# Kernel optimization log

Hardware: AMD Instinct MI355X
Metric: run time of the kernel (lower is better)

Reference implementation:

```python
import jax, jax.numpy as jnp
import numpy as np

# kernel hyperparameters (base_params)
NUGGET = 0.001
REG_LAMBDA = 0.01
FIT_L, FIT_SIGMA = 1.0, 1.0
MMD_L, MMD_SIGMA = 1.0, 1.0
N, D = 4096, 4


def rbf_gram(X1, X2, l, sigma):
    # [N1,N2] radial kernel: sigma^2 * exp(-||x-x'||^2 / (2 l^2)), vectorized
    sq = (jnp.sum(X1 * X1, axis=1)[:, None]
          + jnp.sum(X2 * X2, axis=1)[None, :]
          - 2.0 * (X1 @ X2.T))
    sq = jnp.maximum(sq, 0.0)
    return (sigma * sigma) * jnp.exp(-sq / (2.0 * l * l))


def setup_inputs() -> dict:
    key = jax.random.key(0)
    kx, ky, kz = jax.random.split(key, 3)
    X = jax.random.normal(kx, (N, D), dtype=jnp.float32)
    Y = jax.random.normal(ky, (N, D), dtype=jnp.float32)
    Z = Y + 0.1 * jax.random.normal(kz, (N, D), dtype=jnp.float32)  # Z init'd from Y, perturbed
    return {"X": X, "Y": Y, "Z": Z}


def reference(X, Y, Z):
    # fit_kXX and its nugget-regularized inverse (precomputed in __init__)
    fit_kXX = rbf_gram(X, X, FIT_L, FIT_SIGMA)
    fit_kXX_inv = jnp.linalg.inv(fit_kXX + NUGGET * jnp.eye(X.shape[0], dtype=X.dtype))

    # loss_fit_z: ||k_ZZ||_F^2 - 2 ||k_ZY||_F^2  (torch matrix norm = Frobenius)
    k_ZZ = rbf_gram(Z, Z, MMD_L, MMD_SIGMA)
    k_ZY = rbf_gram(Z, Y, MMD_L, MMD_SIGMA)
    loss_fit = jnp.sum(k_ZZ * k_ZZ) - 2.0 * jnp.sum(k_ZY * k_ZY)

    # loss_reg_z: reg_lambda * trace(Z^T fit_kXX_inv Z)
    loss_reg = REG_LAMBDA * jnp.sum(Z * (fit_kXX_inv @ Z))

    return loss_fit + loss_reg
```

## Files before the change

kernel.cpp:

```cpp
#include <hip/hip_runtime.h>


#define NN 4096
#define LDA 4100
#define OFF_W   ((size_t)NN*LDA)
#define OFF_ACC (OFF_W + (size_t)NN*4)

__device__ __forceinline__ float rdlane(float v, int l){
    return __int_as_float(__builtin_amdgcn_readlane(__float_as_int(v), l));
}

__device__ void wave_chol64(const float* Dm, float* __restrict__ A, int h){
    const int lane = threadIdx.x & 63;
    float row[64];
#pragma unroll
    for (int q=0;q<16;q++){
        float4 v = *(const float4*)(Dm + lane*68 + q*4);
        row[q*4]=v.x; row[q*4+1]=v.y; row[q*4+2]=v.z; row[q*4+3]=v.w;
    }
#pragma unroll
    for (int j=0;j<64;j++){
        float d  = rdlane(row[j], j);
        float sd = sqrtf(d);
        float inv= 1.0f/sd;
        float v  = (lane==j)? sd : row[j]*inv;
        row[j] = v;
#pragma unroll
        for (int c=j+1;c<64;c++){
            float lc = rdlane(v, c);
            row[c] -= v*lc;
        }
    }
#pragma unroll
    for (int q=0;q<16;q++)
        *(float4*)(A + (size_t)(h+lane)*LDA + h + q*4) =
            make_float4(row[q*4],row[q*4+1],row[q*4+2],row[q*4+3]);
}

__global__ void k_build_A(const float* __restrict__ X, float* __restrict__ A){
    const int i  = blockIdx.y;
    const int j0 = (blockIdx.x*256 + threadIdx.x)*4;
    const float4 xi = *(const float4*)(X + (size_t)i*4);
    float out[4];
#pragma unroll
    for (int s=0;s<4;s++){
        const float4 xj = *(const float4*)(X + (size_t)(j0+s)*4);
        float d0=xi.x-xj.x, d1=xi.y-xj.y, d2=xi.z-xj.z, d3=xi.w-xj.w;
        float sq = d0*d0+d1*d1+d2*d2+d3*d3;
        float v  = __expf(-0.5f*sq);
        if (i == j0+s) v += 0.001f;
        out[s]=v;
    }
    *(float4*)(A + (size_t)i*LDA + j0) = make_float4(out[0],out[1],out[2],out[3]);
}

__global__ void k_init(const float* __restrict__ Z, float* __restrict__ W,
                       double* __restrict__ acc){
    const int i = blockIdx.x*256+threadIdx.x;
    ((float4*)W)[i] = ((const float4*)Z)[i];
    if (blockIdx.x==0 && threadIdx.x==0) acc[0]=0.0;
}

__global__ __launch_bounds__(256) void k_chol0(float* __restrict__ A){
    __shared__ float Dm[64*68];
    const int tid = threadIdx.x;
#pragma unroll
    for (int it=0; it<4; ++it){
        int idx = tid + it*256, r = idx>>4, q = idx&15;
        float4 v = *(const float4*)(A + (size_t)r*LDA + q*4);
        *(float4*)&Dm[r*68 + q*4] = v;
    }
    __syncthreads();
    if (tid < 64) wave_chol64(Dm, A, 0);
}

__global__ __launch_bounds__(256) void k_trsm2(float* __restrict__ A, float* __restrict__ W,
                                               int g){
    __shared__ float Ld[64*68];
    __shared__ float dinv[64];
    const int tid = threadIdx.x;
    const int s0  = g*64;
#pragma unroll
    for (int it=0; it<4; ++it){
        int idx = tid + it*256, r = idx>>4, q = idx&15;
        float4 v = *(const float4*)(A + (size_t)(s0+r)*LDA + s0 + q*4);
        *(float4*)&Ld[r*68 + q*4] = v;
    }
    __syncthreads();
    if (tid < 64) dinv[tid] = 1.0f/Ld[tid*68 + tid];
    __syncthreads();

    const int nRB = (66-g)>>2;
    if ((int)blockIdx.x < nRB){
        const int row = s0 + 64 + blockIdx.x*256 + tid;
        const int rl  = row>4095 ? 4095 : row;
        float x[64];
        const float* src = A + (size_t)rl*LDA + s0;
#pragma unroll
        for (int q=0;q<16;q++){
            float4 v = *(const float4*)(src + q*4);
            x[q*4]=v.x; x[q*4+1]=v.y; x[q*4+2]=v.z; x[q*4+3]=v.w;
        }
#pragma unroll
        for (int c=0;c<64;c++){
            float xc = x[c]*dinv[c];
            x[c] = xc;
#pragma unroll
            for (int t=c+1;t<64;t++) x[t] -= xc*Ld[t*68 + c];
        }
        if (row < 4096){
            float* dst = A + (size_t)row*LDA + s0;
#pragma unroll
            for (int q=0;q<16;q++)
                *(float4*)(dst + q*4) = make_float4(x[q*4],x[q*4+1],x[q*4+2],x[q*4+3]);
        }
    } else {
        if (tid < 64){
            const int lane = tid;
            float4 wv = *(const float4*)(W + (size_t)(s0+lane)*4);
            float w0=wv.x, w1=wv.y, w2=wv.z, w3=wv.w;
#pragma unroll
            for (int j=0;j<64;j++){
                if (lane==j){ float dj=dinv[j]; w0*=dj; w1*=dj; w2*=dj; w3*=dj; }
                float b0=__shfl(w0,j), b1=__shfl(w1,j), b2=__shfl(w2,j), b3=__shfl(w3,j);
                float l = Ld[lane*68 + j];
                if (lane>j){ w0-=l*b0; w1-=l*b1; w2-=l*b2; w3-=l*b3; }
            }
            *(float4*)(W + (size_t)(s0+lane)*4) = make_float4(w0,w1,w2,w3);
        }
    }
}

__global__ __launch_bounds__(256) void k_pupd(float* __restrict__ A, float* __restrict__ W,
                                              int g){
    __shared__ float Sh[2*4352];
    const int tid = threadIdx.x;
    const int g64 = g*64;
    const int i = g&3, ncols = 3-i;
    int idx = blockIdx.x;
    int c_blk=-1, r_blk=-1;
#pragma unroll
    for (int cc=0; cc<3; ++cc){
        if (cc < ncols && c_blk < 0){
            int cb = g+1+cc, cnt = 64-cb;
            if (idx < cnt){ c_blk=cb; r_blk=cb+idx; }
            else idx -= cnt;
        }
    }
    const int tx = tid&15, ty = tid>>4;

    if (c_blk >= 0){
        float* PrT = Sh;
        float* PcT = (r_blk==c_blk) ? Sh : (Sh + 4352);
        const int r0 = r_blk*64, c0 = c_blk*64;
#pragma unroll
        for (int it=0; it<4; ++it){
            int ix = tid + it*256, r = ix>>4, q = ix&15;
            float4 v = *(const float4*)(A + (size_t)(r0+r)*LDA + g64 + q*4);
            PrT[(q*4+0)*68+r]=v.x; PrT[(q*4+1)*68+r]=v.y;
            PrT[(q*4+2)*68+r]=v.z; PrT[(q*4+3)*68+r]=v.w;
        }
        if (r_blk != c_blk){
#pragma unroll
            for (int it=0; it<4; ++it){
                int ix = tid + it*256, r = ix>>4, q = ix&15;
                float4 v = *(const float4*)(A + (size_t)(c0+r)*LDA + g64 + q*4);
                PcT[(q*4+0)*68+r]=v.x; PcT[(q*4+1)*68+r]=v.y;
                PcT[(q*4+2)*68+r]=v.z; PcT[(q*4+3)*68+r]=v.w;
            }
        }
        __syncthreads();
        float acc[4][4]={};
#pragma unroll 8
        for (int t=0;t<64;t++){
            float4 a = *(const float4*)&PrT[t*68 + ty*4];
            float4 b = *(const float4*)&PcT[t*68 + tx*4];
            acc[0][0]+=a.x*b.x; acc[0][1]+=a.x*b.y; acc[0][2]+=a.x*b.z; acc[0][3]+=a.x*b.w;
            acc[1][0]+=a.y*b.x; acc[1][1]+=a.y*b.y; acc[1][2]+=a.y*b.z; acc[1][3]+=a.y*b.w;
            acc[2][0]+=a.z*b.x; acc[2][1]+=a.z*b.y; acc[2][2]+=a.z*b.z; acc[2][3]+=a.z*b.w;
            acc[3][0]+=a.w*b.x; acc[3][1]+=a.w*b.y; acc[3][2]+=a.w*b.z; acc[3][3]+=a.w*b.w;
        }
        if (r_blk==c_blk && c_blk==g+1){
            float* Dm = Sh + 4352;
            __syncthreads();
#pragma unroll
            for (int ii=0;ii<4;ii++){
                float4 c = *(const float4*)(A + (size_t)(r0+ty*4+ii)*LDA + c0 + tx*4);
                c.x-=acc[ii][0]; c.y-=acc[ii][1]; c.z-=acc[ii][2]; c.w-=acc[ii][3];
                *(float4*)&Dm[(ty*4+ii)*68 + tx*4] = c;
            }
            __syncthreads();
            if (tid < 64) wave_chol64(Dm, A, r0);
        } else {
#pragma unroll
            for (int ii=0;ii<4;ii++){
                float* p = A + (size_t)(r0+ty*4+ii)*LDA + c0 + tx*4;
                float4 cv = *(float4*)p;
                cv.x-=acc[ii][0]; cv.y-=acc[ii][1]; cv.z-=acc[ii][2]; cv.w-=acc[ii][3];
                *(float4*)p = cv;
            }
        }
    } else {
        const int wr0 = (g+1+idx)*64;
        float* Lt = Sh;
        float* Ws = Sh + 4352;
#pragma unroll
        for (int it=0; it<4; ++it){
            int ix = tid + it*256, r = ix>>4, q = ix&15;
            float4 v = *(const float4*)(A + (size_t)(wr0+r)*LDA + g64 + q*4);
            *(float4*)&Lt[r*68 + q*4] = v;
        }
        if (tid < 64) *(float4*)&Ws[tid*4] = *(const float4*)(W + (size_t)(g64+tid)*4);
        __syncthreads();
        const int row = tid>>2, cw = tid&3;
        float s = 0.f;
#pragma unroll 16
        for (int t=0;t<64;t++) s += Lt[row*68+t]*Ws[t*4+cw];
        float* wp = W + (size_t)(wr0+row)*4 + cw;
        *wp = *wp - s;
    }
}

__global__ __launch_bounds__(256) void k_upd256(float* __restrict__ A, int S){
    __shared__ float S_[8704];
    const int tid = threadIdx.x;
    const int k0 = S*256, base = k0+256;
    const int T2 = (4096-base)>>7;
    const int nT2 = T2*(T2+1)/2;
    const int tx = tid&15, ty = tid>>4;

    if ((int)blockIdx.x == nT2){
        float* PT = S_;
        float* Dm = S_ + 4352;
        float acc[4][4]={};
        for (int kk=0; kk<4; ++kk){
            __syncthreads();
#pragma unroll
            for (int it=0; it<4; ++it){
                int ix = tid + it*256, r = ix>>4, q = ix&15;
                float4 v = *(const float4*)(A + (size_t)(base+r)*LDA + k0 + kk*64 + q*4);
                PT[(q*4+0)*68+r]=v.x; PT[(q*4+1)*68+r]=v.y;
                PT[(q*4+2)*68+r]=v.z; PT[(q*4+3)*68+r]=v.w;
            }
            __syncthreads();
#pragma unroll 8
            for (int t=0;t<64;t++){
                float4 a = *(const float4*)&PT[t*68 + ty*4];
                float4 b = *(const float4*)&PT[t*68 + tx*4];
                acc[0][0]+=a.x*b.x; acc[0][1]+=a.x*b.y; acc[0][2]+=a.x*b.z; acc[0][3]+=a.x*b.w;
                acc[1][0]+=a.y*b.x; acc[1][1]+=a.y*b.y; acc[1][2]+=a.y*b.z; acc[1][3]+=a.y*b.w;
                acc[2][0]+=a.z*b.x; acc[2][1]+=a.z*b.y; acc[2][2]+=a.z*b.z; acc[2][3]+=a.z*b.w;
                acc[3][0]+=a.w*b.x; acc[3][1]+=a.w*b.y; acc[3][2]+=a.w*b.z; acc[3][3]+=a.w*b.w;
            }
        }
        __syncthreads();
#pragma unroll
        for (int ii=0;ii<4;ii++){
            float4 c = *(const float4*)(A + (size_t)(base+ty*4+ii)*LDA + base + tx*4);
            c.x-=acc[ii][0]; c.y-=acc[ii][1]; c.z-=acc[ii][2]; c.w-=acc[ii][3];
            *(float4*)&Dm[(ty*4+ii)*68 + tx*4] = c;
        }
        __syncthreads();
        if (tid < 64) wave_chol64(Dm, A, base);
        return;
    }

    float* Sa = S_;
    float* Sb = S_ + 4224;
    int t2 = blockIdx.x;
    int bi = (int)((sqrtf(8.f*(float)t2+1.f)-1.f)*0.5f);
    while ((bi+1)*(bi+2)/2 <= t2) ++bi;
    while (bi*(bi+1)/2 > t2) --bi;
    const int bj = t2 - bi*(bi+1)/2;
    const int r0 = base + bi*128, c0 = base + bj*128;
    const bool dg = (bi==bj);
    const float* Sbp = dg ? Sa : Sb;
    int row_[4], q_[4];
#pragma unroll
    for (int it=0;it<4;++it){ int ix=tid+it*256; row_[it]=ix>>3; q_[it]=ix&7; }
    float4 ra[4], rb[4];
#pragma unroll
    for (int it=0;it<4;++it){
        ra[it] = *(const float4*)(A + (size_t)(r0+row_[it])*LDA + k0 + q_[it]*4);
        if (!dg) rb[it] = *(const float4*)(A + (size_t)(c0+row_[it])*LDA + k0 + q_[it]*4);
    }
    float acc[8][8]={};
    for (int kk=0;kk<8;++kk){
        __syncthreads();
#pragma unroll
        for (int it=0;it<4;++it){
            Sa[(q_[it]*4+0)*132+row_[it]]=ra[it].x; Sa[(q_[it]*4+1)*132+row_[it]]=ra[it].y;
            Sa[(q_[it]*4+2)*132+row_[it]]=ra[it].z; Sa[(q_[it]*4+3)*132+row_[it]]=ra[it].w;
            if (!dg){
                Sb[(q_[it]*4+0)*132+row_[it]]=rb[it].x; Sb[(q_[it]*4+1)*132+row_[it]]=rb[it].y;
                Sb[(q_[it]*4+2)*132+row_[it]]=rb[it].z; Sb[(q_[it]*4+3)*132+row_[it]]=rb[it].w;
            }
        }
        __syncthreads();
        if (kk < 7){
            const int kb = k0 + (kk+1)*32;
#pragma unroll
            for (int it=0;it<4;++it){
                ra[it] = *(const float4*)(A + (size_t)(r0+row_[it])*LDA + kb + q_[it]*4);
                if (!dg) rb[it] = *(const float4*)(A + (size_t)(c0+row_[it])*LDA + kb + q_[it]*4);
            }
        }
#pragma unroll 4
        for (int t=0;t<32;++t){
            float4 a0 = *(const float4*)&Sa[t*132 + ty*8];
            float4 a1 = *(const float4*)&Sa[t*132 + ty*8 + 4];
            float4 b0 = *(const float4*)&Sbp[t*132 + tx*8];
            float4 b1 = *(const float4*)&Sbp[t*132 + tx*8 + 4];
            float av[8]={a0.x,a0.y,a0.z,a0.w,a1.x,a1.y,a1.z,a1.w};
            float bv[8]={b0.x,b0.y,b0.z,b0.w,b1.x,b1.y,b1.z,b1.w};
#pragma unroll
            for (int ii=0;ii<8;ii++)
#pragma unroll
                for (int jj=0;jj<8;jj++) acc[ii][jj] += av[ii]*bv[jj];
        }
    }
#pragma unroll
    for (int ii=0;ii<8;ii++){
        const int r = r0 + ty*8 + ii;
        const int c = c0 + tx*8;
        if (r < base+64 && c < base+64) continue;
        float* p = A + (size_t)r*LDA + c;
        float4 c1 = *(float4*)p;
        c1.x-=acc[ii][0]; c1.y-=acc[ii][1]; c1.z-=acc[ii][2]; c1.w-=acc[ii][3];
        *(float4*)p = c1;
        float4 c2 = *(float4*)(p+4);
        c2.x-=acc[ii][4]; c2.y-=acc[ii][5]; c2.z-=acc[ii][6]; c2.w-=acc[ii][7];
        *(float4*)(p+4) = c2;
    }
}

__global__ void k_lossfit(const float* __restrict__ Z, const float* __restrict__ Y,
                          double* __restrict__ acc){
    const int tid=threadIdx.x;
    const int i0=blockIdx.x*8;
    double s=0.0;
    for (int ii=0;ii<8;ii++){
        const float4 zi = *(const float4*)(Z + (size_t)(i0+ii)*4);
        for (int j=tid;j<NN;j+=256){
            float4 zj = *(const float4*)(Z + (size_t)j*4);
            float4 yj = *(const float4*)(Y + (size_t)j*4);
            float d0=zi.x-zj.x, d1=zi.y-zj.y, d2=zi.z-zj.z, d3=zi.w-zj.w;
            float dzz = d0*d0+d1*d1+d2*d2+d3*d3;
            d0=zi.x-yj.x; d1=zi.y-yj.y; d2=zi.z-yj.z; d3=zi.w-yj.w;
            float dzy = d0*d0+d1*d1+d2*d2+d3*d3;
            s += (double)(__expf(-dzz) - 2.f*__expf(-dzy));
        }
    }
    for (int o=32;o;o>>=1) s += __shfl_down(s,o);
    __shared__ double ps[4];
    if ((tid&63)==0) ps[tid>>6]=s;
    __syncthreads();
    if (tid==0) atomicAdd(acc, ps[0]+ps[1]+ps[2]+ps[3]);
}

__global__ void k_finish(const float* __restrict__ W, const double* __restrict__ acc,
                         float* __restrict__ out){
    const int tid=threadIdx.x;
    double s=0.0;
    for (int r=tid;r<NN;r+=256){
        float4 v=*(const float4*)(W+(size_t)r*4);
        s += (double)v.x*v.x+(double)v.y*v.y+(double)v.z*v.z+(double)v.w*v.w;
    }
    for (int o=32;o;o>>=1) s += __shfl_down(s,o);
    __shared__ double ps[4];
    if ((tid&63)==0) ps[tid>>6]=s;
    __syncthreads();
    if (tid==0) out[0] = (float)(acc[0] + 0.01*(ps[0]+ps[1]+ps[2]+ps[3]));
}

extern "C" void kernel_launch(void* const* d_in, const int* in_sizes, int n_in,
                              void* d_out, int out_size, void* d_ws, size_t ws_size,
                              hipStream_t stream){
    const float* X=(const float*)d_in[0];
    const float* Y=(const float*)d_in[1];
    const float* Z=(const float*)d_in[2];
    float* ws   = (float*)d_ws;
    float* A    = ws;
    float* W    = ws + OFF_W;
    double* acc = (double*)(ws + OFF_ACC);

    if (ws_size < (OFF_ACC)*sizeof(float) + 16) return;

    k_init   <<<16,256,0,stream>>>(Z, W, acc);
    k_build_A<<<dim3(NN/1024,NN),256,0,stream>>>(X, A);
    k_lossfit<<<512,256,0,stream>>>(Z, Y, acc);
    k_chol0  <<<1,256,0,stream>>>(A);

    for (int g=0; g<64; ++g){
        const int nRB = (66-g)>>2;
        k_trsm2<<<nRB+1,256,0,stream>>>(A, W, g);
        const int i = g&3, ncols = 3-i;
        int ntile = 0;
        for (int cc=0; cc<ncols; ++cc) ntile += 64-(g+1+cc);
        const int nW = 63-g;
        if (ntile+nW > 0) k_pupd<<<ntile+nW,256,0,stream>>>(A, W, g);
        if (i==3 && g<63){
            const int S = g>>2;
            const int T2 = (4096-(S+1)*256)>>7;
            const int nT2 = T2*(T2+1)/2;
            k_upd256<<<nT2+1,256,0,stream>>>(A, S);
        }
    }
    k_finish<<<1,256,0,stream>>>(W, acc, (float*)d_out);
}
```

Baseline: 3.625 ms.

## Fuse blocked Cholesky and triangular solve into one cooperative persistent kernel

Replaces the roughly two hundred per-panel kernel launches (trsm, panel update, 256-wide syrk) with a single cooperative kernel that uses grid-wide syncs between steps. Each diagonal block is factored and also explicitly inverted, so the panel triangular solve becomes a small GEMM against the inverse rather than a serial per-row substitution. The syrk tile layout is also changed to strided column halves. This aims to remove launch overhead and serial trsm latency, at the cost of grid.sync barriers, lower occupancy, and reduced numerical robustness from using an explicit block inverse.

```diff
diff --git a/kernel.cpp b/kernel.cpp
--- a/kernel.cpp
+++ b/kernel.cpp
@@ -1,273 +1,134 @@
 #include <hip/hip_runtime.h>
+#include <hip/hip_cooperative_groups.h>
+namespace cg = cooperative_groups;
 
 
 #define NN 4096
 #define LDA 4100
-#define OFF_W   ((size_t)NN*LDA)
-#define OFF_ACC (OFF_W + (size_t)NN*4)
+#define OFF_W    ((size_t)NN*LDA)
+#define OFF_LI   (OFF_W + (size_t)NN*4)
+#define OFF_ACC  (OFF_LI + 2*4096)
 
 __device__ __forceinline__ float rdlane(float v, int l){
     return __int_as_float(__builtin_amdgcn_readlane(__float_as_int(v), l));
 }
 
-__device__ void wave_chol64(const float* Dm, float* __restrict__ A, int h){
-    const int lane = threadIdx.x & 63;
-    float row[64];
-#pragma unroll
-    for (int q=0;q<16;q++){
-        float4 v = *(const float4*)(Dm + lane*68 + q*4);
-        row[q*4]=v.x; row[q*4+1]=v.y; row[q*4+2]=v.z; row[q*4+3]=v.w;
-    }
-#pragma unroll
-    for (int j=0;j<64;j++){
-        float d  = rdlane(row[j], j);
-        float sd = sqrtf(d);
-        float inv= 1.0f/sd;
-        float v  = (lane==j)? sd : row[j]*inv;
-        row[j] = v;
-#pragma unroll
-        for (int c=j+1;c<64;c++){
-            float lc = rdlane(v, c);
-            row[c] -= v*lc;
-        }
-    }
-#pragma unroll
-    for (int q=0;q<16;q++)
-        *(float4*)(A + (size_t)(h+lane)*LDA + h + q*4) =
-            make_float4(row[q*4],row[q*4+1],row[q*4+2],row[q*4+3]);
-}
-
-__global__ void k_build_A(const float* __restrict__ X, float* __restrict__ A){
-    const int i  = blockIdx.y;
-    const int j0 = (blockIdx.x*256 + threadIdx.x)*4;
-    const float4 xi = *(const float4*)(X + (size_t)i*4);
-    float out[4];
-#pragma unroll
-    for (int s=0;s<4;s++){
-        const float4 xj = *(const float4*)(X + (size_t)(j0+s)*4);
-        float d0=xi.x-xj.x, d1=xi.y-xj.y, d2=xi.z-xj.z, d3=xi.w-xj.w;
-        float sq = d0*d0+d1*d1+d2*d2+d3*d3;
-        float v  = __expf(-0.5f*sq);
-        if (i == j0+s) v += 0.001f;
-        out[s]=v;
-    }
-    *(float4*)(A + (size_t)i*LDA + j0) = make_float4(out[0],out[1],out[2],out[3]);
-}
-
-__global__ void k_init(const float* __restrict__ Z, float* __restrict__ W,
-                       double* __restrict__ acc){
-    const int i = blockIdx.x*256+threadIdx.x;
-    ((float4*)W)[i] = ((const float4*)Z)[i];
-    if (blockIdx.x==0 && threadIdx.x==0) acc[0]=0.0;
-}
-
-__global__ __launch_bounds__(256) void k_chol0(float* __restrict__ A){
-    __shared__ float Dm[64*68];
-    const int tid = threadIdx.x;
+__device__ __forceinline__ void stageT(const float* __restrict__ src, float* __restrict__ dst,
+                                       int tid){
 #pragma unroll
     for (int it=0; it<4; ++it){
         int idx = tid + it*256, r = idx>>4, q = idx&15;
-        float4 v = *(const float4*)(A + (size_t)r*LDA + q*4);
-        *(float4*)&Dm[r*68 + q*4] = v;
-    }
-    __syncthreads();
-    if (tid < 64) wave_chol64(Dm, A, 0);
-}
-
-__global__ __launch_bounds__(256) void k_trsm2(float* __restrict__ A, float* __restrict__ W,
-                                               int g){
-    __shared__ float Ld[64*68];
-    __shared__ float dinv[64];
-    const int tid = threadIdx.x;
-    const int s0  = g*64;
-#pragma unroll
-    for (int it=0; it<4; ++it){
-        int idx = tid + it*256, r = idx>>4, q = idx&15;
-        float4 v = *(const float4*)(A + (size_t)(s0+r)*LDA + s0 + q*4);
-        *(float4*)&Ld[r*68 + q*4] = v;
-    }
-    __syncthreads();
-    if (tid < 64) dinv[tid] = 1.0f/Ld[tid*68 + tid];
-    __syncthreads();
-
-    const int nRB = (66-g)>>2;
-    if ((int)blockIdx.x < nRB){
-        const int row = s0 + 64 + blockIdx.x*256 + tid;
-        const int rl  = row>4095 ? 4095 : row;
-        float x[64];
-        const float* src = A + (size_t)rl*LDA + s0;
+        float4 v = *(const float4*)(src + (size_t)r*LDA + q*4);
+        dst[(q*4+0)*68+r]=v.x; dst[(q*4+1)*68+r]=v.y;
+        dst[(q*4+2)*68+r]=v.z; dst[(q*4+3)*68+r]=v.w;
+    }
+}
+
+__device__ __forceinline__ void gemm_acc(const float* __restrict__ Ab, const float* __restrict__ Bb,
+                                         float acc[4][4], int tx, int ty){
+#pragma unroll 8
+    for (int t=0;t<64;t++){
+        float4 a = *(const float4*)&Ab[t*68 + ty*4];
+        float4 b = *(const float4*)&Bb[t*68 + tx*4];
+        acc[0][0]+=a.x*b.x; acc[0][1]+=a.x*b.y; acc[0][2]+=a.x*b.z; acc[0][3]+=a.x*b.w;
+        acc[1][0]+=a.y*b.x; acc[1][1]+=a.y*b.y; acc[1][2]+=a.y*b.z; acc[1][3]+=a.y*b.w;
+        acc[2][0]+=a.z*b.x; acc[2][1]+=a.z*b.y; acc[2][2]+=a.z*b.z; acc[2][3]+=a.z*b.w;
+        acc[3][0]+=a.w*b.x; acc[3][1]+=a.w*b.y; acc[3][2]+=a.w*b.z; acc[3][3]+=a.w*b.w;
+    }
+}
+
+__device__ void chol_inv_solve(float* S_, float* __restrict__ A, float* __restrict__ W,
+                               float* __restrict__ LTdst, int h, int tid){
+    float* Dm = S_;
+    float* Li = S_ + 4352;
+    float* Ws = S_ + 13056;
+    float* Mt = S_ + 13312;
+    __syncthreads();
+    if (tid < 64){
+        const int lane = tid;
+        float row[64];
 #pragma unroll
         for (int q=0;q<16;q++){
-            float4 v = *(const float4*)(src + q*4);
-            x[q*4]=v.x; x[q*4+1]=v.y; x[q*4+2]=v.z; x[q*4+3]=v.w;
-        }
-#pragma unroll
-        for (int c=0;c<64;c++){
-            float xc = x[c]*dinv[c];
-            x[c] = xc;
-#pragma unroll
-            for (int t=c+1;t<64;t++) x[t] -= xc*Ld[t*68 + c];
-        }
-        if (row < 4096){
-            float* dst = A + (size_t)row*LDA + s0;
-#pragma unroll
-            for (int q=0;q<16;q++)
-                *(float4*)(dst + q*4) = make_float4(x[q*4],x[q*4+1],x[q*4+2],x[q*4+3]);
-        }
-    } else {
-        if (tid < 64){
-            const int lane = tid;
-            float4 wv = *(const float4*)(W + (size_t)(s0+lane)*4);
-            float w0=wv.x, w1=wv.y, w2=wv.z, w3=wv.w;
-#pragma unroll
-            for (int j=0;j<64;j++){
-                if (lane==j){ float dj=dinv[j]; w0*=dj; w1*=dj; w2*=dj; w3*=dj; }
-                float b0=__shfl(w0,j), b1=__shfl(w1,j), b2=__shfl(w2,j), b3=__shfl(w3,j);
-                float l = Ld[lane*68 + j];
-                if (lane>j){ w0-=l*b0; w1-=l*b1; w2-=l*b2; w3-=l*b3; }
-            }
-            *(float4*)(W + (size_t)(s0+lane)*4) = make_float4(w0,w1,w2,w3);
-        }
-    }
-}
-
-__global__ __launch_bounds__(256) void k_pupd(float* __restrict__ A, float* __restrict__ W,
-                                              int g){
-    __shared__ float Sh[2*4352];
-    const int tid = threadIdx.x;
-    const int g64 = g*64;
-    const int i = g&3, ncols = 3-i;
-    int idx = blockIdx.x;
-    int c_blk=-1, r_blk=-1;
-#pragma unroll
-    for (int cc=0; cc<3; ++cc){
-        if (cc < ncols && c_blk < 0){
-            int cb = g+1+cc, cnt = 64-cb;
-            if (idx < cnt){ c_blk=cb; r_blk=cb+idx; }
-            else idx -= cnt;
-        }
-    }
-    const int tx = tid&15, ty = tid>>4;
-
-    if (c_blk >= 0){
-        float* PrT = Sh;
-        float* PcT = (r_blk==c_blk) ? Sh : (Sh + 4352);
-        const int r0 = r_blk*64, c0 = c_blk*64;
-#pragma unroll
-        for (int it=0; it<4; ++it){
-            int ix = tid + it*256, r = ix>>4, q = ix&15;
-            float4 v = *(const float4*)(A + (size_t)(r0+r)*LDA + g64 + q*4);
-            PrT[(q*4+0)*68+r]=v.x; PrT[(q*4+1)*68+r]=v.y;
-            PrT[(q*4+2)*68+r]=v.z; PrT[(q*4+3)*68+r]=v.w;
-        }
-        if (r_blk != c_blk){
-#pragma unroll
-            for (int it=0; it<4; ++it){
-                int ix = tid + it*256, r = ix>>4, q = ix&15;
-                float4 v = *(const float4*)(A + (size_t)(c0+r)*LDA + g64 + q*4);
-                PcT[(q*4+0)*68+r]=v.x; PcT[(q*4+1)*68+r]=v.y;
-                PcT[(q*4+2)*68+r]=v.z; PcT[(q*4+3)*68+r]=v.w;
-            }
-        }
-        __syncthreads();
-        float acc[4][4]={};
-#pragma unroll 8
-        for (int t=0;t<64;t++){
-            float4 a = *(const float4*)&PrT[t*68 + ty*4];
-            float4 b = *(const float4*)&PcT[t*68 + tx*4];
-            acc[0][0]+=a.x*b.x; acc[0][1]+=a.x*b.y; acc[0][2]+=a.x*b.z; acc[0][3]+=a.x*b.w;
-            acc[1][0]+=a.y*b.x; acc[1][1]+=a.y*b.y; acc[1][2]+=a.y*b.z; acc[1][3]+=a.y*b.w;
-            acc[2][0]+=a.z*b.x; acc[2][1]+=a.z*b.y; acc[2][2]+=a.z*b.z; acc[2][3]+=a.z*b.w;
-            acc[3][0]+=a.w*b.x; acc[3][1]+=a.w*b.y; acc[3][2]+=a.w*b.z; acc[3][3]+=a.w*b.w;
-        }
-        if (r_blk==c_blk && c_blk==g+1){
-            float* Dm = Sh + 4352;
-            __syncthreads();
-#pragma unroll
-            for (int ii=0;ii<4;ii++){
-                float4 c = *(const float4*)(A + (size_t)(r0+ty*4+ii)*LDA + c0 + tx*4);
-                c.x-=acc[ii][0]; c.y-=acc[ii][1]; c.z-=acc[ii][2]; c.w-=acc[ii][3];
-                *(float4*)&Dm[(ty*4+ii)*68 + tx*4] = c;
-            }
-            __syncthreads();
-            if (tid < 64) wave_chol64(Dm, A, r0);
-        } else {
-#pragma unroll
-            for (int ii=0;ii<4;ii++){
-                float* p = A + (size_t)(r0+ty*4+ii)*LDA + c0 + tx*4;
-                float4 cv = *(float4*)p;
-                cv.x-=acc[ii][0]; cv.y-=acc[ii][1]; cv.z-=acc[ii][2]; cv.w-=acc[ii][3];
-                *(float4*)p = cv;
-            }
-        }
-    } else {
-        const int wr0 = (g+1+idx)*64;
-        float* Lt = Sh;
-        float* Ws = Sh + 4352;
-#pragma unroll
-        for (int it=0; it<4; ++it){
-            int ix = tid + it*256, r = ix>>4, q = ix&15;
-            float4 v = *(const float4*)(A + (size_t)(wr0+r)*LDA + g64 + q*4);
-            *(float4*)&Lt[r*68 + q*4] = v;
-        }
-        if (tid < 64) *(float4*)&Ws[tid*4] = *(const float4*)(W + (size_t)(g64+tid)*4);
-        __syncthreads();
-        const int row = tid>>2, cw = tid&3;
-        float s = 0.f;
-#pragma unroll 16
-        for (int t=0;t<64;t++) s += Lt[row*68+t]*Ws[t*4+cw];
-        float* wp = W + (size_t)(wr0+row)*4 + cw;
-        *wp = *wp - s;
-    }
-}
-
-__global__ __launch_bounds__(256) void k_upd256(float* __restrict__ A, int S){
-    __shared__ float S_[8704];
-    const int tid = threadIdx.x;
-    const int k0 = S*256, base = k0+256;
-    const int T2 = (4096-base)>>7;
-    const int nT2 = T2*(T2+1)/2;
-    const int tx = tid&15, ty = tid>>4;
-
-    if ((int)blockIdx.x == nT2){
-        float* PT = S_;
-        float* Dm = S_ + 4352;
-        float acc[4][4]={};
-        for (int kk=0; kk<4; ++kk){
-            __syncthreads();
-#pragma unroll
-            for (int it=0; it<4; ++it){
-                int ix = tid + it*256, r = ix>>4, q = ix&15;
-                float4 v = *(const float4*)(A + (size_t)(base+r)*LDA + k0 + kk*64 + q*4);
-                PT[(q*4+0)*68+r]=v.x; PT[(q*4+1)*68+r]=v.y;
-                PT[(q*4+2)*68+r]=v.z; PT[(q*4+3)*68+r]=v.w;
-            }
-            __syncthreads();
-#pragma unroll 8
-            for (int t=0;t<64;t++){
-                float4 a = *(const float4*)&PT[t*68 + ty*4];
-                float4 b = *(const float4*)&PT[t*68 + tx*4];
-                acc[0][0]+=a.x*b.x; acc[0][1]+=a.x*b.y; acc[0][2]+=a.x*b.z; acc[0][3]+=a.x*b.w;
-                acc[1][0]+=a.y*b.x; acc[1][1]+=a.y*b.y; acc[1][2]+=a.y*b.z; acc[1][3]+=a.y*b.w;
-                acc[2][0]+=a.z*b.x; acc[2][1]+=a.z*b.y; acc[2][2]+=a.z*b.z; acc[2][3]+=a.z*b.w;
-                acc[3][0]+=a.w*b.x; acc[3][1]+=a.w*b.y; acc[3][2]+=a.w*b.z; acc[3][3]+=a.w*b.w;
-            }
-        }
-        __syncthreads();
-#pragma unroll
-        for (int ii=0;ii<4;ii++){
-            float4 c = *(const float4*)(A + (size_t)(base+ty*4+ii)*LDA + base + tx*4);
-            c.x-=acc[ii][0]; c.y-=acc[ii][1]; c.z-=acc[ii][2]; c.w-=acc[ii][3];
-            *(float4*)&Dm[(ty*4+ii)*68 + tx*4] = c;
-        }
-        __syncthreads();
-        if (tid < 64) wave_chol64(Dm, A, base);
-        return;
-    }
-
+            float4 v = *(const float4*)&Dm[lane*68 + q*4];
+            row[q*4]=v.x; row[q*4+1]=v.y; row[q*4+2]=v.z; row[q*4+3]=v.w;
+        }
+#pragma unroll
+        for (int j=0;j<64;j++){
+            float d  = rdlane(row[j], j);
+            float sd = sqrtf(d);
+            float iv = 1.0f/sd;
+            float v  = (lane==j)? sd : row[j]*iv;
+            row[j] = v;
+#pragma unroll
+            for (int c=j+1;c<64;c++) row[c] -= v*rdlane(v,c);
+        }
+#pragma unroll
+        for (int q=0;q<16;q++){
+            float4 v = make_float4(row[q*4],row[q*4+1],row[q*4+2],row[q*4+3]);
+            *(float4*)(A + (size_t)(h+lane)*LDA + h + q*4) = v;
+            *(float4*)&Dm[lane*68 + q*4] = v;
+        }
+    }
+    __syncthreads();
+    for (int idx=tid; idx<4096; idx+=256){
+        int r=idx>>6, c=idx&63;
+        if (r<c) Li[r*68+c]=0.f;
+    }
+    __syncthreads();
+    {
+        const int d = tid>>6, cc=(tid>>2)&15, g2=tid&3;
+        const int c = d*16+cc, hi=(d+1)*16;
+        for (int jj=c; jj<hi; ++jj){
+            float part=0.f;
+            for (int t=c+g2; t<jj; t+=4) part += Dm[jj*68+t]*Li[t*68+c];
+            part += __shfl_xor(part,1);
+            part += __shfl_xor(part,2);
+            float x = ((jj==c)?1.f:0.f) - part;
+            x /= Dm[jj*68+jj];
+            if (g2==0) Li[jj*68+c]=x;
+        }
+    }
+    __syncthreads();
+    {
+        const int r16=tid>>4, c16=tid&15;
+        for (int sd2=1; sd2<4; ++sd2){
+            for (int bc=0; bc+sd2<4; ++bc){
+                const int br=bc+sd2;
+                float m=0.f;
+                for (int k=bc;k<br;++k)
+#pragma unroll 4
+                    for (int t2=0;t2<16;t2++)
+                        m += Dm[(16*br+r16)*68+16*k+t2]*Li[(16*k+t2)*68+16*bc+c16];
+                Mt[r16*17+c16]=m;
+                __syncthreads();
+                float x=0.f;
+#pragma unroll 4
+                for (int t=0;t<16;t++)
+                    x += Li[(16*br+r16)*68+16*br+t]*Mt[t*17+c16];
+                __syncthreads();
+                Li[(16*br+r16)*68+16*bc+c16] = -x;
+                __syncthreads();
+            }
+        }
+    }
+    for (int idx=tid; idx<4096; idx+=256){
+        int t=idx>>6, c=idx&63;
+        LTdst[idx] = Li[c*68+t];
+    }
+    if (tid<64) *(float4*)&Ws[tid*4] = *(const float4*)(W + (size_t)(h+tid)*4);
+    __syncthreads();
+    {
+        int i=tid>>2, c=tid&3;
+        float s=0.f;
+        for (int j=0;j<=i;j++) s += Li[i*68+j]*Ws[j*4+c];
+        W[(size_t)(h+i)*4+c] = s;
+    }
+}
+
+__device__ void syrk_tile(float* __restrict__ A, float* S_, int k0, int base, int t2,
+                          int tid, int tx, int ty){
     float* Sa = S_;
-    float* Sb = S_ + 4224;
-    int t2 = blockIdx.x;
+    float* Sb = S_+4224;
     int bi = (int)((sqrtf(8.f*(float)t2+1.f)-1.f)*0.5f);
     while ((bi+1)*(bi+2)/2 <= t2) ++bi;
     while (bi*(bi+1)/2 > t2) --bi;
@@ -309,8 +170,8 @@
         for (int t=0;t<32;++t){
             float4 a0 = *(const float4*)&Sa[t*132 + ty*8];
             float4 a1 = *(const float4*)&Sa[t*132 + ty*8 + 4];
-            float4 b0 = *(const float4*)&Sbp[t*132 + tx*8];
-            float4 b1 = *(const float4*)&Sbp[t*132 + tx*8 + 4];
+            float4 b0 = *(const float4*)&Sbp[t*132 + tx*4];
+            float4 b1 = *(const float4*)&Sbp[t*132 + 64 + tx*4];
             float av[8]={a0.x,a0.y,a0.z,a0.w,a1.x,a1.y,a1.z,a1.w};
             float bv[8]={b0.x,b0.y,b0.z,b0.w,b1.x,b1.y,b1.z,b1.w};
 #pragma unroll
@@ -322,16 +183,173 @@
 #pragma unroll
     for (int ii=0;ii<8;ii++){
         const int r = r0 + ty*8 + ii;
-        const int c = c0 + tx*8;
-        if (r < base+64 && c < base+64) continue;
-        float* p = A + (size_t)r*LDA + c;
-        float4 c1 = *(float4*)p;
-        c1.x-=acc[ii][0]; c1.y-=acc[ii][1]; c1.z-=acc[ii][2]; c1.w-=acc[ii][3];
-        *(float4*)p = c1;
-        float4 c2 = *(float4*)(p+4);
-        c2.x-=acc[ii][4]; c2.y-=acc[ii][5]; c2.z-=acc[ii][6]; c2.w-=acc[ii][7];
-        *(float4*)(p+4) = c2;
-    }
+        const int c1 = c0 + tx*4;
+        const int c2 = c0 + 64 + tx*4;
+        if (!(r < base+64 && c1 < base+64)){
+            float* p = A + (size_t)r*LDA + c1;
+            float4 cv = *(float4*)p;
+            cv.x-=acc[ii][0]; cv.y-=acc[ii][1]; cv.z-=acc[ii][2]; cv.w-=acc[ii][3];
+            *(float4*)p = cv;
+        }
+        if (!(r < base+64 && c2 < base+64)){
+            float* p = A + (size_t)r*LDA + c2;
+            float4 cv = *(float4*)p;
+            cv.x-=acc[ii][4]; cv.y-=acc[ii][5]; cv.z-=acc[ii][6]; cv.w-=acc[ii][7];
+            *(float4*)p = cv;
+        }
+    }
+}
+
+__global__ __launch_bounds__(256,2) void k_coop(float* __restrict__ A, float* __restrict__ W,
+                                                float* __restrict__ LinvTg){
+    cg::grid_group grid = cg::this_grid();
+    __shared__ float S_[13584];
+    const int tid = threadIdx.x;
+    const int bid = blockIdx.x;
+    const int tx = tid&15, ty = tid>>4;
+    float* Ab = S_;
+    float* Bb = S_+4352;
+    float* Iv = S_+8704;
+    float* Ws = S_+13056;
+
+    if (bid==0){
+#pragma unroll
+        for (int it=0; it<4; ++it){
+            int idx=tid+it*256, r=idx>>4, q=idx&15;
+            *(float4*)&Ab[r*68+q*4] = *(const float4*)(A + (size_t)r*LDA + q*4);
+        }
+        chol_inv_solve(S_, A, W, LinvTg, 0, tid);
+    }
+    grid.sync();
+
+    for (int s=0; s<63; ++s){
+        const int S = s>>2;
+        const int scol = s*64;
+        const int nrt = 63 - s;
+        if (bid < nrt){
+            const int r = s+1+bid;
+            const int r64 = r*64;
+            const float* LT = LinvTg + ((s&1)<<12);
+#pragma unroll
+            for (int it=0;it<4;++it){
+                int idx=tid+it*256, t=idx>>4, q=idx&15;
+                *(float4*)&Iv[t*68+q*4] = *(const float4*)(LT + t*64 + q*4);
+            }
+            if (tid<64) *(float4*)&Ws[tid*4] = *(const float4*)(W + (size_t)(scol+tid)*4);
+            float acc[4][4]={};
+            for (int p=4*S; p<s; ++p){
+                __syncthreads();
+                stageT(A + (size_t)r64*LDA + p*64, Ab, tid);
+                stageT(A + (size_t)scol*LDA + p*64, Bb, tid);
+                __syncthreads();
+                gemm_acc(Ab, Bb, acc, tx, ty);
+            }
+            __syncthreads();
+            stageT(A + (size_t)r64*LDA + scol, Ab, tid);
+            __syncthreads();
+#pragma unroll
+            for (int ii=0;ii<4;ii++)
+#pragma unroll
+                for (int jj=0;jj<4;jj++)
+                    Ab[(tx*4+jj)*68 + ty*4+ii] -= acc[ii][jj];
+            __syncthreads();
+            float l[4][4]={};
+            gemm_acc(Ab, Iv, l, tx, ty);
+#pragma unroll
+            for (int ii=0;ii<4;ii++)
+                *(float4*)(A + (size_t)(r64+ty*4+ii)*LDA + scol + tx*4) =
+                    make_float4(l[ii][0],l[ii][1],l[ii][2],l[ii][3]);
+            __syncthreads();
+#pragma unroll
+            for (int ii=0;ii<4;ii++)
+#pragma unroll
+                for (int jj=0;jj<4;jj++)
+                    Bb[(tx*4+jj)*68 + ty*4+ii] = l[ii][jj];
+            __syncthreads();
+            {
+                int i=tid>>2, c=tid&3;
+                float s2=0.f;
+#pragma unroll 16
+                for (int j=0;j<64;j++) s2 += Bb[j*68+i]*Ws[j*4+c];
+                float* wp = W + (size_t)(r64+i)*4 + c;
+                *wp -= s2;
+            }
+            if (r <= 4*S+3){
+                __syncthreads();
+                float dd[4][4]={};
+                gemm_acc(Bb, Bb, dd, tx, ty);
+                if (r == s+1){
+#pragma unroll
+                    for (int ii=0;ii<4;ii++){
+                        float4 c4 = *(const float4*)(A + (size_t)(r64+ty*4+ii)*LDA + r64 + tx*4);
+                        c4.x-=dd[ii][0]; c4.y-=dd[ii][1]; c4.z-=dd[ii][2]; c4.w-=dd[ii][3];
+                        *(float4*)&Ab[(ty*4+ii)*68 + tx*4] = c4;
+                    }
+                    chol_inv_solve(S_, A, W, LinvTg + (((s+1)&1)<<12), r64, tid);
+                } else {
+#pragma unroll
+                    for (int ii=0;ii<4;ii++){
+                        float* p = A + (size_t)(r64+ty*4+ii)*LDA + r64 + tx*4;
+                        float4 c4 = *(float4*)p;
+                        c4.x-=dd[ii][0]; c4.y-=dd[ii][1]; c4.z-=dd[ii][2]; c4.w-=dd[ii][3];
+                        *(float4*)p = c4;
+                    }
+                }
+            }
+        }
+        grid.sync();
+        if ((s&3)==3){
+            const int k0 = S*256, base = k0+256;
+            const int T2 = (4096-base)>>7;
+            const int nT2 = T2*(T2+1)/2;
+            if (bid==0){
+                float acc[4][4]={};
+                for (int kk=0;kk<4;++kk){
+                    __syncthreads();
+                    stageT(A + (size_t)base*LDA + k0 + kk*64, Bb, tid);
+                    __syncthreads();
+                    gemm_acc(Bb, Bb, acc, tx, ty);
+                }
+                __syncthreads();
+#pragma unroll
+                for (int ii=0;ii<4;ii++){
+                    float4 c4 = *(const float4*)(A + (size_t)(base+ty*4+ii)*LDA + base + tx*4);
+                    c4.x-=acc[ii][0]; c4.y-=acc[ii][1]; c4.z-=acc[ii][2]; c4.w-=acc[ii][3];
+                    *(float4*)&Ab[(ty*4+ii)*68 + tx*4] = c4;
+                }
+                chol_inv_solve(S_, A, W, LinvTg, base, tid);
+            } else {
+                const int stride = (int)gridDim.x - 1;
+                for (int t2=bid-1; t2<nT2; t2+=stride)
+                    syrk_tile(A, S_, k0, base, t2, tid, tx, ty);
+            }
+            grid.sync();
+        }
+    }
+}
+
+__global__ void k_build_A(const float* __restrict__ X, float* __restrict__ A){
+    const int i  = blockIdx.y;
+    const int j0 = (blockIdx.x*256 + threadIdx.x)*4;
+    const float4 xi = *(const float4*)(X + (size_t)i*4);
+    float out[4];
+#pragma unroll
+    for (int s=0;s<4;s++){
+        const float4 xj = *(const float4*)(X + (size_t)(j0+s)*4);
+        float d0=xi.x-xj.x, d1=xi.y-xj.y, d2=xi.z-xj.z, d3=xi.w-xj.w;
+        float sq = d0*d0+d1*d1+d2*d2+d3*d3;
+        float v  = __expf(-0.5f*sq);
+        if (i == j0+s) v += 0.001f;
+        out[s]=v;
+    }
+    *(float4*)(A + (size_t)i*LDA + j0) = make_float4(out[0],out[1],out[2],out[3]);
+}
+
+__global__ void k_init(const float* __restrict__ Z, float* __restrict__ W,
+                       double* __restrict__ acc){
+    const int i = blockIdx.x*256+threadIdx.x;
+    ((float4*)W)[i] = ((const float4*)Z)[i];
+    if (blockIdx.x==0 && threadIdx.x==0) acc[0]=0.0;
 }
 
 __global__ void k_lossfit(const float* __restrict__ Z, const float* __restrict__ Y,
@@ -382,29 +400,21 @@
     float* ws   = (float*)d_ws;
     float* A    = ws;
     float* W    = ws + OFF_W;
+    float* Li   = ws + OFF_LI;
     double* acc = (double*)(ws + OFF_ACC);
 
-    if (ws_size < (OFF_ACC)*sizeof(float) + 16) return;
+    if (ws_size < (OFF_ACC+4)*sizeof(float)) return;
 
     k_init   <<<16,256,0,stream>>>(Z, W, acc);
-    k_build_A<<<dim3(NN/1024,NN),256,0,stream>>>(X, A);
+    k_build_A<<<dim3(4,NN),256,0,stream>>>(X, A);
     k_lossfit<<<512,256,0,stream>>>(Z, Y, acc);
-    k_chol0  <<<1,256,0,stream>>>(A);
-
-    for (int g=0; g<64; ++g){
-        const int nRB = (66-g)>>2;
-        k_trsm2<<<nRB+1,256,0,stream>>>(A, W, g);
-        const int i = g&3, ncols = 3-i;
-        int ntile = 0;
-        for (int cc=0; cc<ncols; ++cc) ntile += 64-(g+1+cc);
-        const int nW = 63-g;
-        if (ntile+nW > 0) k_pupd<<<ntile+nW,256,0,stream>>>(A, W, g);
-        if (i==3 && g<63){
-            const int S = g>>2;
-            const int T2 = (4096-(S+1)*256)>>7;
-            const int nT2 = T2*(T2+1)/2;
-            k_upd256<<<nT2+1,256,0,stream>>>(A, S);
-        }
-    }
+
+    int nb = 0;
+    hipOccupancyMaxActiveBlocksPerMultiprocessor(&nb, (const void*)k_coop, 256, 0);
+    if (nb < 1) nb = 1;
+    int gridc = nb*256; if (gridc > 512) gridc = 512;
+    void* args[] = { (void*)&A, (void*)&W, (void*)&Li };
+    hipLaunchCooperativeKernel((const void*)k_coop, dim3(gridc), dim3(256), args, 0, stream);
+
     k_finish<<<1,256,0,stream>>>(W, acc, (float*)d_out);
 }
```

After: 6.052 ms. 67.0% more time.
